# Optimization experiments

Hardware: AMD Instinct MI355X
Metric: run time of the kernel (lower is better)

The kernel has to match this reference:

```python
import jax, jax.numpy as jnp
import numpy as np

EPS = 1e-5  # nn.LayerNorm default


def typed_linear(x, types, W):
    # DGL TypedLinear: y_i = x_i @ W[type_i]; W: (T, in, out). T is small -> loop over types.
    out = jnp.zeros((x.shape[0], W.shape[2]), x.dtype)
    for t in range(W.shape[0]):
        out = jnp.where((types == t)[:, None], x @ W[t], out)
    return out


def layer_norm(x, g, b):
    mu = jnp.mean(x, axis=-1, keepdims=True)
    var = jnp.mean((x - mu) ** 2, axis=-1, keepdims=True)
    return (x - mu) * jax.lax.rsqrt(var + EPS) * g + b


def setup_inputs() -> dict:
    key = jax.random.key(0)
    ks = jax.random.split(key, 16)
    N, E, D, H, Dh, T, C = 20000, 320000, 128, 8, 16, 3, 64
    s = 0.05
    return {
        "x": jax.random.normal(ks[0], (N, D), jnp.float32),
        "global_context": jax.random.normal(ks[1], (C,), jnp.float32),
        "Wk": jax.random.normal(ks[2], (T, D, H * Dh), jnp.float32) * s,
        "Wq": jax.random.normal(ks[3], (T, D, H * Dh), jnp.float32) * s,
        "Wv": jax.random.normal(ks[4], (T, D, H * Dh), jnp.float32) * s,
        "rel_att": jax.random.normal(ks[5], (H, Dh, Dh), jnp.float32) * s,
        "rel_msg": jax.random.normal(ks[6], (H, Dh, Dh), jnp.float32) * s,
        "rel_pri": jnp.ones((H,), jnp.float32),
        "Wa": jax.random.normal(ks[7], (T, H * Dh, H * Dh), jnp.float32) * s,
        "skip": jnp.ones((T,), jnp.float32),
        "ln_g": jnp.ones((H * Dh,), jnp.float32),
        "ln_b": jnp.zeros((H * Dh,), jnp.float32),
        "film_w": jax.random.normal(ks[8], (C, 2 * D), jnp.float32) * s,
        "film_b": jnp.zeros((2 * D,), jnp.float32),
        "ntype": jax.random.randint(ks[9], (N,), 0, T, jnp.int32),
        "src": jax.random.randint(ks[10], (E,), 0, N, jnp.int32),
        "dst": jax.random.randint(ks[11], (E,), 0, N, jnp.int32),
    }


def reference(x, global_context, Wk, Wq, Wv, rel_att, rel_msg, rel_pri, Wa,
              skip, ln_g, ln_b, film_w, film_b, ntype, src, dst):
    N, D = x.shape
    H, Dh, _ = rel_att.shape
    inv_sqrt_d = 1.0 / jnp.sqrt(jnp.asarray(Dh, x.dtype))

    # Per-node-type K/Q/V projections
    k = typed_linear(x, ntype, Wk).reshape(N, H, Dh)
    q = typed_linear(x, ntype, Wq).reshape(N, H, Dh)
    v = typed_linear(x, ntype, Wv).reshape(N, H, Dh)

    # Per-edge attention score & message (num_etypes == 1 -> single relation matrices)
    kw = jnp.einsum('ehd,hdo->eho', k[src], rel_att)                 # (E,H,Dh)
    a = jnp.einsum('eho,eho->eh', kw, q[dst]) * rel_pri * inv_sqrt_d  # (E,H)
    m = jnp.einsum('ehd,hdo->eho', v[src], rel_msg)                  # (E,H,Dh)

    # Edge softmax grouped by destination node
    amax = jax.ops.segment_max(a, dst, num_segments=N)               # (N,H)
    ae = jnp.exp(a - amax[dst])
    asum = jax.ops.segment_sum(ae, dst, num_segments=N)
    attn = ae / asum[dst]

    # Scatter-add aggregation
    h_agg = jax.ops.segment_sum(m * attn[..., None], dst, num_segments=N).reshape(N, H * Dh)

    # Target-specific output projection + gated residual + LayerNorm (use_norm=True)
    h = typed_linear(h_agg, ntype, Wa)
    alpha = jax.nn.sigmoid(skip)[ntype][:, None]
    h = h * alpha + x * (1.0 - alpha)
    h = layer_norm(h, ln_g, ln_b)

    # Outer skip (Identity: in_dim == out_dim) + FiLM modulation by global context
    h = h + x
    gb = global_context @ film_w + film_b
    gamma, beta = gb[:D], gb[D:]
    return gamma[None, :] * h + beta[None, :]
```

## Files before the change

### kernel.cpp

```cpp
#include <hip/hip_runtime.h>
#include <hip/hip_bf16.h>

constexpr int D  = 128;
constexpr int H  = 8;
constexpr int DH = 16;
constexpr int NB  = 16;
constexpr int NBO = 16;
constexpr int T  = 3;

typedef __attribute__((ext_vector_type(8))) short bf16x8;
typedef __attribute__((ext_vector_type(4))) float f32x4;

__device__ inline unsigned short f2bf(float f) {
  unsigned u = __float_as_uint(f);
  unsigned r = u + 0x7fffu + ((u >> 16) & 1u);
  return (unsigned short)(r >> 16);
}

__global__ void k_prep(const int* __restrict__ dst, const int* __restrict__ ntype,
                       int* __restrict__ deg, int* __restrict__ tcnt, int N, int E,
                       const float* __restrict__ x, unsigned short* __restrict__ xb,
                       int n8,
                       const float* __restrict__ Wk, const float* __restrict__ Wq,
                       const float* __restrict__ Wv, unsigned short* __restrict__ Wt,
                       const float* __restrict__ ra_, const float* __restrict__ rm_,
                       const float* __restrict__ rp,
                       const float* __restrict__ gc, const float* __restrict__ fw,
                       const float* __restrict__ fb, float* __restrict__ gb, int C,
                       int BE) {
  int blk = blockIdx.x, tid = threadIdx.x;
  if (blk == 0) {
    float a0 = 0.f, a1 = 0.f, a2 = 0.f, a3 = 0.f;
    int c = 0;
    for (; c + 4 <= C; c += 4) {
      a0 += gc[c] * fw[c * 256 + tid];
      a1 += gc[c + 1] * fw[(c + 1) * 256 + tid];
      a2 += gc[c + 2] * fw[(c + 2) * 256 + tid];
      a3 += gc[c + 3] * fw[(c + 3) * 256 + tid];
    }
    float acc = fb[tid] + (a0 + a1) + (a2 + a3);
    for (; c < C; ++c) acc += gc[c] * fw[c * 256 + tid];
    gb[tid] = acc;
    return;
  }
  if (blk < 73) {
    int b2 = blk - 1;
    int mt = b2 >> 3, chunk = b2 & 7;
    int m = mt / T, t = mt % T;
    unsigned short* o = Wt + ((size_t)m * T + t) * (D * D);
    if (m == 0) {
      const float* W = Wk + (size_t)t * (D * D);
#pragma unroll
      for (int k2 = 0; k2 < 8; ++k2) {
        int idx = k2 * 256 + tid;
        int d = idx & 127, colL = idx >> 7;
        int col = chunk * 16 + colL;
        o[(size_t)col * D + d] = f2bf(W[(size_t)d * D + col]);
      }
      return;
    }
    __shared__ float cf[256];
    int h = chunk;
    if (m == 1) cf[tid] = ra_[h * 256 + tid];
    else        cf[tid] = rm_[h * 256 + (tid & 15) * 16 + (tid >> 4)];
    float scale = (m == 1) ? rp[h] * 0.25f : 1.f;
    __syncthreads();
    const float* W = (m == 1 ? Wq : Wv) + (size_t)t * (D * D);
#pragma unroll
    for (int k2 = 0; k2 < 8; ++k2) {
      int idx = k2 * 256 + tid;
      int c = idx & 127, colL = idx >> 7;
      int col = chunk * 16 + colL, dd = colL;
      const float* wrow = W + (size_t)c * D + h * 16;
      float s = 0.f;
#pragma unroll
      for (int z = 0; z < 16; ++z) s += wrow[z] * cf[dd * 16 + z];
      o[(size_t)col * D + c] = f2bf(s * scale);
    }
    return;
  }
  if (blk < 73 + BE) {
    int base = (blk - 73) * 1024;
    int lane = tid & 63;
#pragma unroll
    for (int k2 = 0; k2 < 4; ++k2) {
      int i = base + k2 * 256 + tid;
      if (i < E) atomicAdd(deg + dst[i], 1);
      int t = (i < N) ? ntype[i] : -1;
#pragma unroll
      for (int tt = 0; tt < T; ++tt) {
        unsigned long long mask = __ballot(t == tt);
        int cnt = __popcll(mask);
        if (cnt > 0 && lane == (__ffsll((long long)mask) - 1))
          atomicAdd(tcnt + tt, cnt);
      }
    }
    return;
  }
  int i = (blk - 73 - BE) * 256 + tid;
  if (i >= n8) return;
  const float4* p = (const float4*)(x + (size_t)i * 8);
  float4 a = p[0], b = p[1];
  ushort4 o0 = {f2bf(a.x), f2bf(a.y), f2bf(a.z), f2bf(a.w)};
  ushort4 o1 = {f2bf(b.x), f2bf(b.y), f2bf(b.z), f2bf(b.w)};
  ushort4* q = (ushort4*)(xb + (size_t)i * 8);
  q[0] = o0;
  q[1] = o1;
}

__global__ void k_scan(const int* __restrict__ deg, int* __restrict__ off,
                       const int* __restrict__ tcnt, int* __restrict__ toff,
                       int N, int E) {
  __shared__ int wsum[16];
  __shared__ int base_s;
  int tid = threadIdx.x;
  int lane = tid & 63, w = tid >> 6;
  if (tid == 0) {
    base_s = 0;
    toff[0] = 0;
    for (int t = 0; t < T; ++t) toff[t + 1] = toff[t] + ((tcnt[t] + NB - 1) / NB) * NB;
  }
  __syncthreads();
  for (int start = 0; start < N; start += 1024) {
    int i = start + tid;
    int v = (i < N) ? deg[i] : 0;
    int x = v;
#pragma unroll
    for (int o = 1; o < 64; o <<= 1) {
      int y = __shfl_up(x, o);
      if (lane >= o) x += y;
    }
    if (lane == 63) wsum[w] = x;
    __syncthreads();
    if (w == 0 && lane < 16) {
      int s = wsum[lane];
#pragma unroll
      for (int o = 1; o < 16; o <<= 1) {
        int y = __shfl_up(s, o);
        if (lane >= o) s += y;
      }
      wsum[lane] = s;
    }
    __syncthreads();
    int waveoff = (w > 0) ? wsum[w - 1] : 0;
    if (i < N) off[i] = base_s + waveoff + x - v;
    __syncthreads();
    if (tid == 0) base_s += wsum[15];
    __syncthreads();
  }
  if (tid == 0) off[N] = E;
}

__global__ void k_scatter(const int* __restrict__ dst, const int* __restrict__ src,
                          const int* __restrict__ ntype,
                          const int* __restrict__ off, const int* __restrict__ toff,
                          int* __restrict__ cursor, int* __restrict__ tcur,
                          int* __restrict__ esrc, int* __restrict__ pnid, int N, int E) {
  int i = blockIdx.x * blockDim.x + threadIdx.x;
  if (i < E) {
    int d = dst[i];
    int pos = atomicAdd(cursor + d, 1);
    esrc[off[d] + pos] = src[i];
  }
  int t = (i < N) ? ntype[i] : -1;
  int lane = threadIdx.x & 63;
#pragma unroll
  for (int tt = 0; tt < T; ++tt) {
    unsigned long long mask = __ballot(t == tt);
    int cnt = __popcll(mask);
    if (cnt == 0) continue;
    int leader = __ffsll((long long)mask) - 1;
    int base = 0;
    if (lane == leader) base = atomicAdd(tcur + tt, cnt);
    base = __shfl(base, leader);
    if (t == tt) {
      int rank = __popcll(mask & ((1ull << lane) - 1ull));
      pnid[toff[tt] + base + rank] = i;
    }
  }
}

__global__ void __launch_bounds__(256)
k_proj_f(const unsigned short* __restrict__ xb, const int* __restrict__ pnid,
         const int* __restrict__ ntype, const unsigned short* __restrict__ Wt,
         unsigned int* __restrict__ kmpk, float* __restrict__ oqt) {
  int b = blockIdx.x;
  int tid = threadIdx.x;
  int w = tid >> 6, l = tid & 63;
  __shared__ int nid_s[NB];
  if (tid < NB) nid_s[tid] = pnid[b * NB + tid];
  __syncthreads();
  int tfirst = -1;
#pragma unroll
  for (int nn = 0; nn < NB; ++nn) if (tfirst < 0 && nid_s[nn] >= 0) tfirst = ntype[nid_s[nn]];
  if (tfirst < 0) return;

  int arow = l & 15, kg = l >> 4;
  int anid = nid_s[arow];
  if (anid < 0) anid = 0;
  const unsigned short* abase = xb + (size_t)anid * D + kg * 8;
  int col0 = w * 32 + (l & 15);
  size_t coff = (size_t)col0 * D + kg * 8;
  const unsigned short* wk = Wt + ((size_t)0 * T + tfirst) * (D * D) + coff;
  const unsigned short* wq = Wt + ((size_t)1 * T + tfirst) * (D * D) + coff;
  const unsigned short* wv = Wt + ((size_t)2 * T + tfirst) * (D * D) + coff;
  f32x4 aK0 = {0.f, 0.f, 0.f, 0.f}, aK1 = aK0;
  f32x4 aQ0 = aK0, aQ1 = aK0, aV0 = aK0, aV1 = aK0;
#pragma unroll
  for (int ks = 0; ks < 4; ++ks) {
    bf16x8 af  = *(const bf16x8*)(abase + ks * 32);
    bf16x8 k0  = *(const bf16x8*)(wk + ks * 32);
    bf16x8 k1  = *(const bf16x8*)(wk + (size_t)16 * D + ks * 32);
    bf16x8 q0  = *(const bf16x8*)(wq + ks * 32);
    bf16x8 q1  = *(const bf16x8*)(wq + (size_t)16 * D + ks * 32);
    bf16x8 v0  = *(const bf16x8*)(wv + ks * 32);
    bf16x8 v1  = *(const bf16x8*)(wv + (size_t)16 * D + ks * 32);
    aK0 = __builtin_amdgcn_mfma_f32_16x16x32_bf16(af, k0, aK0, 0, 0, 0);
    aK1 = __builtin_amdgcn_mfma_f32_16x16x32_bf16(af, k1, aK1, 0, 0, 0);
    aQ0 = __builtin_amdgcn_mfma_f32_16x16x32_bf16(af, q0, aQ0, 0, 0, 0);
    aQ1 = __builtin_amdgcn_mfma_f32_16x16x32_bf16(af, q1, aQ1, 0, 0, 0);
    aV0 = __builtin_amdgcn_mfma_f32_16x16x32_bf16(af, v0, aV0, 0, 0, 0);
    aV1 = __builtin_amdgcn_mfma_f32_16x16x32_bf16(af, v1, aV1, 0, 0, 0);
  }

  int o = l & 15, kg4 = (l >> 4) * 4;
#pragma unroll
  for (int ct = 0; ct < 2; ++ct) {
    f32x4 aK = ct ? aK1 : aK0;
    f32x4 aQ = ct ? aQ1 : aQ0;
    f32x4 aV = ct ? aV1 : aV0;
    int col = w * 32 + ct * 16 + o;
#pragma unroll
    for (int r = 0; r < 4; ++r) {
      int nid = nid_s[kg4 + r];
      if (nid >= 0) {
        kmpk[(size_t)nid * D + col] =
            ((unsigned)f2bf(aV[r]) << 16) | (unsigned)f2bf(aK[r]);
        oqt[(size_t)nid * D + col] = aQ[r];
      }
    }
  }
}

__global__ void k_agg(const int* __restrict__ esrc, const int* __restrict__ off,
                      const unsigned int* __restrict__ kmpk,
                      const float* __restrict__ qt,
                      float* __restrict__ hagg, int N) {
  int n = blockIdx.x;
  int j = threadIdx.x;
  float qv = qt[(size_t)n * D + j];
  int i0 = off[n], i1 = off[n + 1];
  float ssum = 0.f, acc = 0.f;
  int i = i0;
  for (; i + 4 <= i1; i += 4) {
    int s0 = esrc[i], s1 = esrc[i + 1], s2 = esrc[i + 2], s3 = esrc[i + 3];
    unsigned p0 = kmpk[(size_t)s0 * D + j];
    unsigned p1 = kmpk[(size_t)s1 * D + j];
    unsigned p2 = kmpk[(size_t)s2 * D + j];
    unsigned p3 = kmpk[(size_t)s3 * D + j];
    float kv0 = __uint_as_float(p0 << 16), mv0 = __uint_as_float(p0 & 0xffff0000u);
    float kv1 = __uint_as_float(p1 << 16), mv1 = __uint_as_float(p1 & 0xffff0000u);
    float kv2 = __uint_as_float(p2 << 16), mv2 = __uint_as_float(p2 & 0xffff0000u);
    float kv3 = __uint_as_float(p3 << 16), mv3 = __uint_as_float(p3 & 0xffff0000u);
    float a0 = kv0 * qv, a1 = kv1 * qv, a2 = kv2 * qv, a3 = kv3 * qv;
#pragma unroll
    for (int o = 8; o >= 1; o >>= 1) {
      a0 += __shfl_xor(a0, o);
      a1 += __shfl_xor(a1, o);
      a2 += __shfl_xor(a2, o);
      a3 += __shfl_xor(a3, o);
    }
    float w0 = __expf(a0), w1 = __expf(a1), w2 = __expf(a2), w3 = __expf(a3);
    ssum += (w0 + w1) + (w2 + w3);
    acc += (w0 * mv0 + w1 * mv1) + (w2 * mv2 + w3 * mv3);
  }
  for (; i < i1; ++i) {
    int sn = esrc[i];
    unsigned p = kmpk[(size_t)sn * D + j];
    float kv = __uint_as_float(p << 16), mv = __uint_as_float(p & 0xffff0000u);
    float a = kv * qv;
#pragma unroll
    for (int o = 8; o >= 1; o >>= 1) a += __shfl_xor(a, o);
    float wgt = __expf(a);
    ssum += wgt;
    acc += wgt * mv;
  }
  hagg[(size_t)n * D + j] = (ssum > 0.f) ? acc / ssum : 0.f;
}

__global__ void __launch_bounds__(512)
k_out(const float* __restrict__ hagg, const int* __restrict__ pnid,
      const int* __restrict__ ntype, const float* __restrict__ Wa,
      const float* __restrict__ x, const float* __restrict__ skip,
      const float* __restrict__ ln_g, const float* __restrict__ ln_b,
      const float* __restrict__ gb, float* __restrict__ out) {
  int b = blockIdx.x, tid = threadIdx.x;
  int j = tid & 127, g = tid >> 7;
  __shared__ __align__(16) float hs[NBO][D];
  __shared__ int nid_s[NBO];
  __shared__ float red[8][4][2];
  if (tid < NBO) nid_s[tid] = pnid[b * NBO + tid];
  __syncthreads();
  for (int idx = tid; idx < NBO * D; idx += 512) {
    int nn = idx >> 7, col = idx & 127;
    int nid = nid_s[nn];
    hs[nn][col] = (nid >= 0) ? hagg[(size_t)nid * D + col] : 0.f;
  }
  __syncthreads();
  int tfirst = -1;
#pragma unroll
  for (int nn = 0; nn < NBO; ++nn) if (tfirst < 0 && nid_s[nn] >= 0) tfirst = ntype[nid_s[nn]];
  if (tfirst < 0) return;
  float xpre[4];
#pragma unroll
  for (int nn = 0; nn < 4; ++nn) {
    int nid = nid_s[g * 4 + nn];
    xpre[nn] = (nid >= 0) ? x[(size_t)nid * D + j] : 0.f;
  }
  const float* wp = Wa + (size_t)tfirst * (D * D) + j;
  float acc[4];
#pragma unroll
  for (int nn = 0; nn < 4; ++nn) acc[nn] = 0.f;
#pragma unroll 4
  for (int d = 0; d < D; d += 4) {
    float w0 = wp[(size_t)d * D];
    float w1 = wp[(size_t)(d + 1) * D];
    float w2 = wp[(size_t)(d + 2) * D];
    float w3 = wp[(size_t)(d + 3) * D];
#pragma unroll
    for (int nn = 0; nn < 4; ++nn) {
      float4 h4 = *(const float4*)(&hs[g * 4 + nn][d]);
      acc[nn] = fmaf(h4.x, w0, acc[nn]);
      acc[nn] = fmaf(h4.y, w1, acc[nn]);
      acc[nn] = fmaf(h4.z, w2, acc[nn]);
      acc[nn] = fmaf(h4.w, w3, acc[nn]);
    }
  }
  float alpha = 1.f / (1.f + __expf(-skip[tfirst]));
  int w = tid >> 6;
  float hv[4];
#pragma unroll
  for (int nn = 0; nn < 4; ++nn) {
    int nid = nid_s[g * 4 + nn];
    hv[nn] = (nid >= 0) ? (acc[nn] * alpha + xpre[nn] * (1.f - alpha)) : 0.f;
    float s1 = hv[nn], s2 = hv[nn] * hv[nn];
#pragma unroll
    for (int o = 1; o < 64; o <<= 1) {
      s1 += __shfl_xor(s1, o);
      s2 += __shfl_xor(s2, o);
    }
    if ((tid & 63) == 0) { red[w][nn][0] = s1; red[w][nn][1] = s2; }
  }
  __syncthreads();
  float gj = ln_g[j], bj = ln_b[j], gmj = gb[j], gbj = gb[D + j];
#pragma unroll
  for (int nn = 0; nn < 4; ++nn) {
    int nid = nid_s[g * 4 + nn];
    if (nid < 0) continue;
    float mu = (red[2 * g][nn][0] + red[2 * g + 1][nn][0]) * (1.f / D);
    float m2 = (red[2 * g][nn][1] + red[2 * g + 1][nn][1]) * (1.f / D);
    float var = m2 - mu * mu;
    float y = (hv[nn] - mu) * rsqrtf(var + 1e-5f) * gj + bj + xpre[nn];
    out[(size_t)nid * D + j] = gmj * y + gbj;
  }
}

extern "C" void kernel_launch(void* const* d_in, const int* in_sizes, int n_in,
                              void* d_out, int out_size, void* d_ws, size_t ws_size,
                              hipStream_t stream) {
  const float* x       = (const float*)d_in[0];
  const float* gc      = (const float*)d_in[1];
  const float* Wk      = (const float*)d_in[2];
  const float* Wq      = (const float*)d_in[3];
  const float* Wv      = (const float*)d_in[4];
  const float* rel_att = (const float*)d_in[5];
  const float* rel_msg = (const float*)d_in[6];
  const float* rel_pri = (const float*)d_in[7];
  const float* Wa      = (const float*)d_in[8];
  const float* skip    = (const float*)d_in[9];
  const float* ln_g    = (const float*)d_in[10];
  const float* ln_b    = (const float*)d_in[11];
  const float* fw      = (const float*)d_in[12];
  const float* fb      = (const float*)d_in[13];
  const int* ntype     = (const int*)d_in[14];
  const int* src       = (const int*)d_in[15];
  const int* dst       = (const int*)d_in[16];
  float* out = (float*)d_out;

  int N = in_sizes[0] / D;
  int C = in_sizes[1];
  int E = in_sizes[15];

  int gridP = (N + NB - 1) / NB + T;
  int P = gridP * NB;
  int gridO = P / NBO;

  float* ws = (float*)d_ws;
  size_t nD = (size_t)N * D;
  float* wqt   = ws;
  float* whagg = wqt + nD;
  float* wgb   = whagg + nD;
  unsigned int*   kmpk = (unsigned int*)(wgb + 256);
  unsigned short* xb   = (unsigned short*)(kmpk + nD);
  unsigned short* Wt   = xb + nD;
  int* deg    = (int*)(Wt + 9 * D * D);
  int* cursor = deg + N;
  int* tcnt   = cursor + N;
  int* tcur   = tcnt + T;
  int* off    = tcur + T;
  int* toff   = off + N + 1;
  int* esrc   = toff + T + 1;
  int* pnid   = esrc + E;

  (void)hipMemsetAsync(deg, 0, (size_t)(2 * N + 2 * T) * sizeof(int), stream);
  (void)hipMemsetAsync(pnid, 0xFF, (size_t)P * sizeof(int), stream);

  int mNE = (E > N) ? E : N;
  int n8 = (int)(nD / 8);
  int BE = (mNE + 1023) / 1024;
  int BX = (n8 + 255) / 256;
  k_prep<<<73 + BE + BX, 256, 0, stream>>>(dst, ntype, deg, tcnt, N, E,
                                           x, xb, n8, Wk, Wq, Wv, Wt,
                                           rel_att, rel_msg, rel_pri,
                                           gc, fw, fb, wgb, C, BE);
  k_scan<<<1, 1024, 0, stream>>>(deg, off, tcnt, toff, N, E);
  k_scatter<<<(mNE + 255) / 256, 256, 0, stream>>>(dst, src, ntype, off, toff,
                                                   cursor, tcur, esrc, pnid, N, E);
  k_proj_f<<<gridP, 256, 0, stream>>>(xb, pnid, ntype, Wt, kmpk, wqt);
  k_agg<<<N, D, 0, stream>>>(esrc, off, kmpk, wqt, whagg, N);
  k_out<<<gridO, 512, 0, stream>>>(whagg, pnid, ntype, Wa, x, skip, ln_g, ln_b,
                                   wgb, out);
}
```

Measured before the change: 173.0 us.

## Replace single-block degree scan with multi-block atomic segment allocation

The serial one-block exclusive scan over node degrees is replaced by a grid-wide kernel. Each wave does a local prefix sum and claims a base offset with one atomicAdd on a global cursor. The CSR segments are therefore no longer ordered by node id, so the aggregation kernel computes each segment end from off plus deg instead of off[n+1]. This removes a long serial kernel from the critical path, at the cost of nondeterministic segment placement and possibly less locality in edge reads.

New measurement: 156.3 us. -9.6%, faster.

```diff
diff --git a/kernel.cpp b/kernel.cpp
--- a/kernel.cpp
+++ b/kernel.cpp
@@ -108,47 +108,27 @@
   q[1] = o1;
 }
 
-__global__ void k_scan(const int* __restrict__ deg, int* __restrict__ off,
-                       const int* __restrict__ tcnt, int* __restrict__ toff,
-                       int N, int E) {
-  __shared__ int wsum[16];
-  __shared__ int base_s;
-  int tid = threadIdx.x;
-  int lane = tid & 63, w = tid >> 6;
-  if (tid == 0) {
-    base_s = 0;
+__global__ void k_alloc(const int* __restrict__ deg, int* __restrict__ off,
+                        const int* __restrict__ tcnt, int* __restrict__ toff,
+                        int* __restrict__ ecur, int N) {
+  int i = blockIdx.x * blockDim.x + threadIdx.x;
+  int lane = threadIdx.x & 63;
+  if (blockIdx.x == 0 && threadIdx.x == 0) {
     toff[0] = 0;
     for (int t = 0; t < T; ++t) toff[t + 1] = toff[t] + ((tcnt[t] + NB - 1) / NB) * NB;
   }
-  __syncthreads();
-  for (int start = 0; start < N; start += 1024) {
-    int i = start + tid;
-    int v = (i < N) ? deg[i] : 0;
-    int x = v;
-#pragma unroll
-    for (int o = 1; o < 64; o <<= 1) {
-      int y = __shfl_up(x, o);
-      if (lane >= o) x += y;
-    }
-    if (lane == 63) wsum[w] = x;
-    __syncthreads();
-    if (w == 0 && lane < 16) {
-      int s = wsum[lane];
-#pragma unroll
-      for (int o = 1; o < 16; o <<= 1) {
-        int y = __shfl_up(s, o);
-        if (lane >= o) s += y;
-      }
-      wsum[lane] = s;
-    }
-    __syncthreads();
-    int waveoff = (w > 0) ? wsum[w - 1] : 0;
-    if (i < N) off[i] = base_s + waveoff + x - v;
-    __syncthreads();
-    if (tid == 0) base_s += wsum[15];
-    __syncthreads();
-  }
-  if (tid == 0) off[N] = E;
+  int v = (i < N) ? deg[i] : 0;
+  int xs = v;
+#pragma unroll
+  for (int o = 1; o < 64; o <<= 1) {
+    int y = __shfl_up(xs, o);
+    if (lane >= o) xs += y;
+  }
+  int wtotal = __shfl(xs, 63);
+  int base = 0;
+  if (lane == 63) base = atomicAdd(ecur, wtotal);
+  base = __shfl(base, 63);
+  if (i < N) off[i] = base + xs - v;
 }
 
 __global__ void k_scatter(const int* __restrict__ dst, const int* __restrict__ src,
@@ -243,13 +223,14 @@
 }
 
 __global__ void k_agg(const int* __restrict__ esrc, const int* __restrict__ off,
+                      const int* __restrict__ deg,
                       const unsigned int* __restrict__ kmpk,
                       const float* __restrict__ qt,
                       float* __restrict__ hagg, int N) {
   int n = blockIdx.x;
   int j = threadIdx.x;
   float qv = qt[(size_t)n * D + j];
-  int i0 = off[n], i1 = off[n + 1];
+  int i0 = off[n], i1 = i0 + deg[n];
   float ssum = 0.f, acc = 0.f;
   int i = i0;
   for (; i + 4 <= i1; i += 4) {
@@ -407,12 +388,13 @@
   int* cursor = deg + N;
   int* tcnt   = cursor + N;
   int* tcur   = tcnt + T;
-  int* off    = tcur + T;
-  int* toff   = off + N + 1;
+  int* ecur   = tcur + T;
+  int* off    = ecur + 1;
+  int* toff   = off + N;
   int* esrc   = toff + T + 1;
   int* pnid   = esrc + E;
 
-  (void)hipMemsetAsync(deg, 0, (size_t)(2 * N + 2 * T) * sizeof(int), stream);
+  (void)hipMemsetAsync(deg, 0, (size_t)(2 * N + 2 * T + 1) * sizeof(int), stream);
   (void)hipMemsetAsync(pnid, 0xFF, (size_t)P * sizeof(int), stream);
 
   int mNE = (E > N) ? E : N;
@@ -423,11 +405,11 @@
                                            x, xb, n8, Wk, Wq, Wv, Wt,
                                            rel_att, rel_msg, rel_pri,
                                            gc, fw, fb, wgb, C, BE);
-  k_scan<<<1, 1024, 0, stream>>>(deg, off, tcnt, toff, N, E);
+  k_alloc<<<(N + 255) / 256, 256, 0, stream>>>(deg, off, tcnt, toff, ecur, N);
   k_scatter<<<(mNE + 255) / 256, 256, 0, stream>>>(dst, src, ntype, off, toff,
                                                    cursor, tcur, esrc, pnid, N, E);
   k_proj_f<<<gridP, 256, 0, stream>>>(xb, pnid, ntype, Wt, kmpk, wqt);
-  k_agg<<<N, D, 0, stream>>>(esrc, off, kmpk, wqt, whagg, N);
+  k_agg<<<N, D, 0, stream>>>(esrc, off, deg, kmpk, wqt, whagg, N);
   k_out<<<gridO, 512, 0, stream>>>(whagg, pnid, ntype, Wa, x, skip, ln_g, ln_b,
                                    wgb, out);
 }
```
